# Kernel tuning notes

Hardware: AMD Instinct MI355X
Metric: run time of the kernel (lower is better)

Reference implementation:

```python
import jax, jax.numpy as jnp
import numpy as np

N = 100000          # total nodes (ground + sub)
G = 50000           # ground nodes (first G)
E = 800000          # edges per edge set
H = 64              # hidden_features
F_IN = 32           # node_features
MAX_DEG = 20        # MFConv max_degree
NUM_GRAPHS = 128
DEPTH = 1
LN_EPS = 1e-5


def setup_inputs() -> dict:
    key = jax.random.key(0)
    ks = jax.random.split(key, 12)

    def edges(k):
        return jax.random.randint(k, (2, E), 0, N, dtype=jnp.int32)

    return {
        "x": jax.random.normal(ks[0], (N, F_IN), jnp.float32),
        "edge_index": edges(ks[1]),
        "subgraph_edge_index": edges(ks[2]),
        "node_subnode_index": edges(ks[3]),
        "subnode_node_index": edges(ks[4]),
        "ground_node": jnp.arange(N) < G,
        "subgraph_batch_index": jax.random.randint(ks[5], (N - G,), 0, NUM_GRAPHS, dtype=jnp.int32),
        "batch_idx": jax.random.randint(ks[6], (N,), 0, NUM_GRAPHS, dtype=jnp.int32),
        # learned parameters
        "emb_w": jax.random.normal(ks[7], (F_IN, H), jnp.float32) / np.sqrt(F_IN).astype(np.float32),
        "emb_b": jnp.zeros((H,), jnp.float32),
        # 4 MFConvs per depth, 21 degree buckets each; lins_l has bias, lins_r has none
        "conv_wl": jax.random.normal(ks[8], (DEPTH, 4, MAX_DEG + 1, H, H), jnp.float32) / np.sqrt(H).astype(np.float32),
        "conv_bl": jnp.zeros((DEPTH, 4, MAX_DEG + 1, H), jnp.float32),
        "conv_wr": jax.random.normal(ks[9], (DEPTH, 4, MAX_DEG + 1, H, H), jnp.float32) / np.sqrt(H).astype(np.float32),
        "ln_g": jnp.ones((DEPTH, H), jnp.float32),
        "ln_b": jnp.zeros((DEPTH, H), jnp.float32),
        "out_w": jax.random.normal(ks[10], (H, 1), jnp.float32) / np.sqrt(H).astype(np.float32),
        "out_b": jnp.zeros((1,), jnp.float32),
    }


def _mfconv(x, ei, wl, bl, wr):
    """PyG MFConv: out_i = lins_l[deg_i](sum_{j->i} x_j) + lins_r[deg_i](x_i).
    Returns (out, update_mask) where update_mask marks nodes receiving >=1 message
    (catch_lone_sender equivalent)."""
    src, dst = ei[0], ei[1]
    n = x.shape[0]
    deg = jax.ops.segment_sum(jnp.ones(src.shape, jnp.float32), dst, num_segments=n)
    d = jnp.minimum(deg.astype(jnp.int32), MAX_DEG)
    h = jax.ops.segment_sum(x[src], dst, num_segments=n)      # [N, H] neighbor sum
    out = jnp.zeros_like(x)
    for k in range(MAX_DEG + 1):                              # fixed 21 degree buckets
        m = (d == k)[:, None]
        out = out + jnp.where(m, h @ wl[k] + bl[k] + x @ wr[k], 0.0)
    return out, deg > 0


def _layernorm(h, g, b):
    mu = jnp.mean(h, axis=-1, keepdims=True)
    var = jnp.mean(jnp.square(h - mu), axis=-1, keepdims=True)
    return (h - mu) * jax.lax.rsqrt(var + LN_EPS) * g + b


def reference(x, edge_index, subgraph_edge_index, node_subnode_index,
              subnode_node_index, ground_node, subgraph_batch_index, batch_idx,
              emb_w, emb_b, conv_wl, conv_bl, conv_wr, ln_g, ln_b, out_w, out_b):
    h = x @ emb_w + emb_b                                     # embedding
    eis = (edge_index, node_subnode_index, subgraph_edge_index, subnode_node_index)
    for i in range(DEPTH):
        if i != 0:
            h = jax.nn.relu(h)
        h0 = h                                                # residual skip
        for j, ei in enumerate(eis):
            out, upd = _mfconv(h, ei, conv_wl[i, j], conv_bl[i, j], conv_wr[i, j])
            h = jnp.where(upd[:, None], out, h)               # masking=True restore
            if j < 3:
                h = jax.nn.relu(h)
        h = _layernorm(h, ln_g[i], ln_b[i])
        h = h + h0
    # global_add_pool over ground nodes only
    pooled = jax.ops.segment_sum(jnp.where(ground_node[:, None], h, 0.0),
                                 batch_idx, num_segments=NUM_GRAPHS)
    return pooled @ out_w + out_b
```

## Files before the change

kernel.cpp:

```cpp
#include <hip/hip_runtime.h>

#define N_NODES 100000
#define G_NODES 50000
#define N_EDGES 800000
#define H 64
#define F_IN 32
#define MAX_DEG 20
#define NUM_GRAPHS 128
#define LN_EPS 1e-5f
#define POOL_BLOCKS 256
#define MAX_TILES 1600

#define NBINS 512
#define BPB 782
#define BINCAP_LOG 13
#define BINCAP 8192
#define CHUNK 6250
#define MKEYS (4 * N_NODES)
#define MEDGES (4 * N_EDGES)

typedef __attribute__((ext_vector_type(8))) short short8;
typedef __attribute__((ext_vector_type(4))) float float4v;

static __device__ __forceinline__ unsigned short f2b(float f) {
  unsigned u = __float_as_uint(f);
  return (unsigned short)((u + 0x7fffu + ((u >> 16) & 1u)) >> 16);
}
static __device__ __forceinline__ float b2f(unsigned short b) {
  return __uint_as_float(((unsigned)b) << 16);
}

__global__ __launch_bounds__(256) void wconv_kernel(
    const float* __restrict__ wl, const float* __restrict__ wr,
    const float* __restrict__ ew, unsigned short* __restrict__ wbt,
    unsigned short* __restrict__ ewbt, int* __restrict__ bincur,
    int* __restrict__ bcnt) {
  int i = blockIdx.x * 256 + threadIdx.x;
  if (blockIdx.x == 0) {
    for (int k = threadIdx.x; k < NBINS; k += 256) bincur[k] = k << BINCAP_LOG;
    if (threadIdx.x < 84) bcnt[threadIdx.x] = 0;
  }
  if (i < 84 * 64 * 128) {
    int k = i & 127;
    int ch = (i >> 7) & 63;
    int jb = i >> 13;
    float v = (k < 64) ? wl[jb * 4096 + k * 64 + ch]
                       : wr[jb * 4096 + (k - 64) * 64 + ch];
    wbt[i] = f2b(v);
  } else if (i < 84 * 64 * 128 + H * F_IN) {
    int ii = i - 84 * 64 * 128;
    int c = ii >> 5, f = ii & 31;
    ewbt[ii] = f2b(ew[f * H + c]);
  }
}

__global__ __launch_bounds__(256) void emb_kernel(
    const float* __restrict__ x, const unsigned short* __restrict__ ewbt,
    const float* __restrict__ eb, float* __restrict__ h0,
    unsigned short* __restrict__ ab, float* __restrict__ pooled) {
  int tid = threadIdx.x;
  if (blockIdx.x == 0) {
    for (int i = tid; i < NUM_GRAPHS * H; i += 256) pooled[i] = 0.f;
  }
  int base = blockIdx.x * 64;
  int nIn = min(64, N_NODES - base);
  int qw = tid >> 6, lane = tid & 63;
  __shared__ unsigned short aL[64 * 40];
  __shared__ float outF[64 * 68];

  {
    int node = tid >> 2, chb = (tid & 3) * 8;
    unsigned short v8[8];
    if (node < nIn) {
      const float* xr = x + ((size_t)(base + node)) * F_IN + chb;
      float4 f0 = *(const float4*)(xr);
      float4 f1 = *(const float4*)(xr + 4);
      v8[0] = f2b(f0.x); v8[1] = f2b(f0.y); v8[2] = f2b(f0.z); v8[3] = f2b(f0.w);
      v8[4] = f2b(f1.x); v8[5] = f2b(f1.y); v8[6] = f2b(f1.z); v8[7] = f2b(f1.w);
    } else {
#pragma unroll
      for (int i = 0; i < 8; ++i) v8[i] = 0;
    }
    *(short8*)&aL[(tid >> 2) * 40 + chb] = *(short8*)v8;
  }

  int m = lane & 15, quad = lane >> 4;
  short8 a = *(const short8*)&aL[(qw * 16 + m) * 40 + quad * 8];
  float4v acc[4];
#pragma unroll
  for (int t = 0; t < 4; ++t) {
    float bv = eb[t * 16 + m];
    acc[t] = (float4v){bv, bv, bv, bv};
  }
#pragma unroll
  for (int t = 0; t < 4; ++t) {
    short8 bf = *(const short8*)&ewbt[(t * 16 + m) * F_IN + quad * 8];
    acc[t] = __builtin_amdgcn_mfma_f32_16x16x32_bf16(a, bf, acc[t], 0, 0, 0);
  }
#pragma unroll
  for (int t = 0; t < 4; ++t)
#pragma unroll
    for (int r = 0; r < 4; ++r)
      outF[(qw * 16 + quad * 4 + r) * 68 + t * 16 + m] = acc[t][r];
  for (int r = qw * 16; r < qw * 16 + 16; ++r) {
    if (r < nIn) {
      int node = base + r;
      float v = outF[r * 68 + lane];
      if (node < G_NODES) h0[node * H + lane] = v;
      ab[node * 128 + 64 + lane] = f2b(v);
    }
  }
}

__global__ __launch_bounds__(1024) void p3_binscatter(
    const int* __restrict__ e0, const int* __restrict__ e1,
    const int* __restrict__ e2, const int* __restrict__ e3,
    int* __restrict__ bincur, unsigned* __restrict__ binned) {
  __shared__ int hist[NBINS];
  __shared__ int loff[NBINS];
  __shared__ int gcur[NBINS];
  __shared__ int lcur[NBINS];
  __shared__ int wtot[16];
  __shared__ int lmeta[CHUNK];
  __shared__ unsigned sbuf[CHUNK];
  __shared__ unsigned short sbin[CHUNK];
  int t = threadIdx.x, b = blockIdx.x;
  for (int i = t; i < NBINS; i += 1024) hist[i] = 0;
  __syncthreads();
  int j = b >> 7;
  const int* ei = (j == 0) ? e0 : (j == 1) ? e1 : (j == 2) ? e2 : e3;
  int ebase = (b & 127) * CHUNK;
  for (int i = t; i < CHUNK; i += 1024) {
    int dst = ei[N_EDGES + ebase + i];
    int key = j * N_NODES + dst;
    int bin = key / BPB;
    lmeta[i] = (bin << 10) | (key - bin * BPB);
    atomicAdd(&hist[bin], 1);
  }
  __syncthreads();
  int v = (t < NBINS) ? hist[t] : 0;
  int incl = v;
#pragma unroll
  for (int off = 1; off < 64; off <<= 1) {
    int y = __shfl_up(incl, off, 64);
    if ((t & 63) >= off) incl += y;
  }
  if (t < NBINS && (t & 63) == 63) wtot[t >> 6] = incl;
  __syncthreads();
  if (t < NBINS) {
    int wbase = 0;
    for (int w = 0; w < (t >> 6); ++w) wbase += wtot[w];
    int ex = wbase + incl - v;
    loff[t] = ex;
    lcur[t] = ex;
    gcur[t] = v ? atomicAdd(&bincur[t], v) : 0;
  }
  __syncthreads();
  for (int i = t; i < CHUNK; i += 1024) {
    int src = ei[ebase + i];
    int m = lmeta[i];
    int bin = m >> 10;
    int pos = atomicAdd(&lcur[bin], 1);
    sbuf[pos] = ((unsigned)(m & 1023) << 17) | (unsigned)src;
    sbin[pos] = (unsigned short)bin;
  }
  __syncthreads();
  for (int i = t; i < CHUNK; i += 1024) {
    int bb = sbin[i];
    binned[gcur[bb] + (i - loff[bb])] = sbuf[i];
  }
}

__global__ __launch_bounds__(1024) void p46_kernel(
    const unsigned* __restrict__ binned, const int* __restrict__ bincur,
    int* __restrict__ deg4, int* __restrict__ S, int* __restrict__ slots,
    int* __restrict__ bcnt) {
  __shared__ int hist[BPB];
  __shared__ int cur[BPB];
  __shared__ int bh[84];
  __shared__ int wtot[16];
  __shared__ unsigned bufin[BINCAP];
  __shared__ int bufout[BINCAP];
  int t = threadIdx.x, bin = blockIdx.x;
  int kb = bin * BPB;
  for (int i = t; i < BPB; i += 1024) hist[i] = 0;
  if (t < 84) bh[t] = 0;
  __syncthreads();
  int start = bin << BINCAP_LOG;
  int end = bincur[bin];
  int n = end - start;
  for (int i = t; i < n; i += 1024) {
    unsigned v = binned[start + i];
    bufin[i] = v;
    atomicAdd(&hist[v >> 17], 1);
  }
  __syncthreads();
  for (int i = t; i < BPB; i += 1024) {
    int key = kb + i;
    if (key < MKEYS) {
      int d = hist[i];
      deg4[key] = d;
      int j = key / N_NODES;
      int b = d < MAX_DEG ? d : MAX_DEG;
      atomicAdd(&bh[j * 21 + b], 1);
    }
  }
  int base = t * 4;
  int v0 = 0, v1 = 0, v2 = 0, v3 = 0;
  if (base < BPB) {
    v0 = hist[base];
    v1 = (base + 1 < BPB) ? hist[base + 1] : 0;
    v2 = (base + 2 < BPB) ? hist[base + 2] : 0;
    v3 = (base + 3 < BPB) ? hist[base + 3] : 0;
  }
  int s = v0 + v1 + v2 + v3;
  int incl = s;
#pragma unroll
  for (int off = 1; off < 64; off <<= 1) {
    int y = __shfl_up(incl, off, 64);
    if ((t & 63) >= off) incl += y;
  }
  if ((t & 63) == 63) wtot[t >> 6] = incl;
  __syncthreads();
  int wbase = 0;
  for (int w = 0; w < (t >> 6); ++w) wbase += wtot[w];
  int ex = wbase + incl - s;
  if (base < BPB) {
    cur[base] = ex;
    if (base + 1 < BPB) cur[base + 1] = ex + v0;
    if (base + 2 < BPB) cur[base + 2] = ex + v0 + v1;
    if (base + 3 < BPB) cur[base + 3] = ex + v0 + v1 + v2;
  }
  __syncthreads();
  for (int i = t; i < BPB; i += 1024)
    if (kb + i < MKEYS) S[kb + i] = start + cur[i];
  if (t < 84 && bh[t]) atomicAdd(&bcnt[t], bh[t]);
  __syncthreads();
  for (int i = t; i < n; i += 1024) {
    unsigned v = bufin[i];
    int pos = atomicAdd(&cur[v >> 17], 1);
    bufout[pos] = (int)(v & 0x1ffffu);
  }
  __syncthreads();
  for (int i = t; i < n; i += 1024) slots[start + i] = bufout[i];
}

__global__ __launch_bounds__(128) void bucket_scan(
    const int* __restrict__ bcnt, int* __restrict__ boff, int* __restrict__ bcur,
    int* __restrict__ ntiles, int* __restrict__ tdesc) {
  __shared__ int wt[2];
  __shared__ int exL[84], cntL[84], toffL[84];
  int t = threadIdx.x;
  int v = (t < 84) ? bcnt[t] : 0;
  int incl = v;
#pragma unroll
  for (int off = 1; off < 64; off <<= 1) {
    int y = __shfl_up(incl, off, 64);
    if ((t & 63) >= off) incl += y;
  }
  if ((t & 63) == 63) wt[t >> 6] = incl;
  __syncthreads();
  int wbase = (t >> 6) ? wt[0] : 0;
  if (t < 84) {
    int ex = wbase + incl - v;
    boff[t] = ex;
    bcur[t] = ex;
    exL[t] = ex;
    cntL[t] = v;
  }
  __syncthreads();
  if (t < 4) {
    int acc = 0;
    for (int bb = 0; bb < 21; ++bb) {
      toffL[t * 21 + bb] = acc;
      acc += (cntL[t * 21 + bb] + 63) >> 6;
    }
    ntiles[t] = acc;
  }
  __syncthreads();
  for (int jb = 0; jb < 84; ++jb) {
    int j = jb / 21, b = jb - j * 21;
    int cnt = cntL[jb], off = exL[jb], tb = toffL[jb];
    int nt = (cnt + 63) >> 6;
    for (int i = t; i < nt; i += 128) {
      int s2 = i << 6;
      int nIn = min(64, cnt - s2);
      tdesc[j * MAX_TILES + tb + i] = ((off + s2) << 12) | (b << 7) | nIn;
    }
  }
}

__global__ __launch_bounds__(256) void bucket_fill(
    const int* __restrict__ deg4, int* __restrict__ bcur, int* __restrict__ blist) {
  __shared__ int hist[21];
  __shared__ int base[21];
  int t = threadIdx.x;
  if (t < 21) hist[t] = 0;
  __syncthreads();
  int node = blockIdx.x * 256 + t;
  int j = blockIdx.y;
  int b = 0, lpos = 0;
  bool valid = (node < N_NODES);
  if (valid) {
    int d = deg4[j * N_NODES + node];
    b = d < MAX_DEG ? d : MAX_DEG;
    lpos = atomicAdd(&hist[b], 1);
  }
  __syncthreads();
  if (t < 21 && hist[t]) base[t] = atomicAdd(&bcur[j * 21 + t], hist[t]);
  __syncthreads();
  if (valid) blist[base[b] + lpos] = node;
}

__global__ __launch_bounds__(256) void conv_kernel(
    float* __restrict__ h, unsigned short* __restrict__ ab,
    const int* __restrict__ S, const int* __restrict__ deg,
    const int* __restrict__ slots,
    const int* __restrict__ blist, const int* __restrict__ tdesc,
    const int* __restrict__ ntiles, const unsigned short* __restrict__ wbt,
    const float* __restrict__ bl, int j, int inoff, int do_relu, int last) {
  if ((int)blockIdx.x >= ntiles[j]) return;
  int d = tdesc[j * MAX_TILES + blockIdx.x];
  int nIn = d & 127;
  int b = (d >> 7) & 31;
  const int* lst = blist + (d >> 12);
  int outoff = 64 - inoff;

  int tid = threadIdx.x;
  int qw = tid >> 6, lane = tid & 63;

  if (b == 0) {
    for (int r = qw * 16; r < qw * 16 + 16; ++r) {
      if (r < nIn) {
        int node = lst[r];
        float v = b2f(ab[node * 128 + inoff + lane]);
        if (do_relu) v = fmaxf(v, 0.f);
        if (last) {
          if (node < G_NODES) h[node * H + lane] = v;
        } else {
          ab[node * 128 + outoff + lane] = f2b(v);
        }
      }
    }
    return;
  }

  __shared__ unsigned short aL[64 * 136];
  __shared__ int nodeS[64];

  {
    int r = tid >> 2;
    int cb = (tid & 3) * 16;
    bool act = (r < nIn);
    int node = act ? lst[r] : 0;
    if ((tid & 3) == 0 && act) nodeS[r] = node;

    float acc[16];
#pragma unroll
    for (int k = 0; k < 16; ++k) acc[k] = 0.f;
    uint4 selfA = make_uint4(0u, 0u, 0u, 0u);
    uint4 selfB = make_uint4(0u, 0u, 0u, 0u);

#define ACC8(v, kb)                                                      \
  acc[kb + 0] += b2f((unsigned short)(v).x);                             \
  acc[kb + 1] += b2f((unsigned short)((v).x >> 16));                     \
  acc[kb + 2] += b2f((unsigned short)(v).y);                             \
  acc[kb + 3] += b2f((unsigned short)((v).y >> 16));                     \
  acc[kb + 4] += b2f((unsigned short)(v).z);                             \
  acc[kb + 5] += b2f((unsigned short)((v).z >> 16));                     \
  acc[kb + 6] += b2f((unsigned short)(v).w);                             \
  acc[kb + 7] += b2f((unsigned short)((v).w >> 16));

    if (act) {
      const unsigned short* abb = ab + inoff + cb;
      selfA = *(const uint4*)&abb[node * 128];
      selfB = *(const uint4*)&abb[node * 128 + 8];
      int off = S[node];
      int dg = (b < MAX_DEG) ? b : deg[node];
      int e = 0;
      for (; e + 3 < dg; e += 4) {
        int n0 = slots[off + e];
        int n1 = slots[off + e + 1];
        int n2 = slots[off + e + 2];
        int n3 = slots[off + e + 3];
        uint4 a0 = *(const uint4*)&abb[n0 * 128];
        uint4 b0 = *(const uint4*)&abb[n0 * 128 + 8];
        uint4 a1 = *(const uint4*)&abb[n1 * 128];
        uint4 b1 = *(const uint4*)&abb[n1 * 128 + 8];
        uint4 a2 = *(const uint4*)&abb[n2 * 128];
        uint4 b2 = *(const uint4*)&abb[n2 * 128 + 8];
        uint4 a3 = *(const uint4*)&abb[n3 * 128];
        uint4 b3 = *(const uint4*)&abb[n3 * 128 + 8];
        ACC8(a0, 0) ACC8(b0, 8)
        ACC8(a1, 0) ACC8(b1, 8)
        ACC8(a2, 0) ACC8(b2, 8)
        ACC8(a3, 0) ACC8(b3, 8)
      }
      int rem = dg - e;
      if (rem > 0) {
        int n0 = slots[off + e];
        int n1 = (rem > 1) ? slots[off + e + 1] : n0;
        int n2 = (rem > 2) ? slots[off + e + 2] : n0;
        uint4 a0 = *(const uint4*)&abb[n0 * 128];
        uint4 b0 = *(const uint4*)&abb[n0 * 128 + 8];
        uint4 a1 = *(const uint4*)&abb[n1 * 128];
        uint4 b1 = *(const uint4*)&abb[n1 * 128 + 8];
        uint4 a2 = *(const uint4*)&abb[n2 * 128];
        uint4 b2 = *(const uint4*)&abb[n2 * 128 + 8];
        ACC8(a0, 0) ACC8(b0, 8)
        if (rem > 1) { ACC8(a1, 0) ACC8(b1, 8) }
        if (rem > 2) { ACC8(a2, 0) ACC8(b2, 8) }
      }
    }
#undef ACC8

    unsigned p0 = (unsigned)f2b(acc[0]) | ((unsigned)f2b(acc[1]) << 16);
    unsigned p1 = (unsigned)f2b(acc[2]) | ((unsigned)f2b(acc[3]) << 16);
    unsigned p2 = (unsigned)f2b(acc[4]) | ((unsigned)f2b(acc[5]) << 16);
    unsigned p3 = (unsigned)f2b(acc[6]) | ((unsigned)f2b(acc[7]) << 16);
    unsigned p4 = (unsigned)f2b(acc[8]) | ((unsigned)f2b(acc[9]) << 16);
    unsigned p5 = (unsigned)f2b(acc[10]) | ((unsigned)f2b(acc[11]) << 16);
    unsigned p6 = (unsigned)f2b(acc[12]) | ((unsigned)f2b(acc[13]) << 16);
    unsigned p7 = (unsigned)f2b(acc[14]) | ((unsigned)f2b(acc[15]) << 16);
    *(uint4*)&aL[r * 136 + cb] = make_uint4(p0, p1, p2, p3);
    *(uint4*)&aL[r * 136 + cb + 8] = make_uint4(p4, p5, p6, p7);
    *(uint4*)&aL[r * 136 + 64 + cb] = selfA;
    *(uint4*)&aL[r * 136 + 64 + cb + 8] = selfB;
  }

  int m = lane & 15, quad = lane >> 4;
  const unsigned short* wbase = wbt + (size_t)(j * 21 + b) * 64 * 128;
  float4v acc[4];
#pragma unroll
  for (int t = 0; t < 4; ++t) {
    float bv = bl[b * 64 + t * 16 + m];
    acc[t] = (float4v){bv, bv, bv, bv};
  }
#pragma unroll
  for (int ks = 0; ks < 4; ++ks) {
    short8 a = *(const short8*)&aL[(qw * 16 + m) * 136 + ks * 32 + quad * 8];
#pragma unroll
    for (int t = 0; t < 4; ++t) {
      short8 bf = *(const short8*)&wbase[(t * 16 + m) * 128 + ks * 32 + quad * 8];
      acc[t] = __builtin_amdgcn_mfma_f32_16x16x32_bf16(a, bf, acc[t], 0, 0, 0);
    }
  }
  if (do_relu) {
#pragma unroll
    for (int t = 0; t < 4; ++t)
#pragma unroll
      for (int r = 0; r < 4; ++r) acc[t][r] = fmaxf(acc[t][r], 0.f);
  }
  float* outF = (float*)aL;
#pragma unroll
  for (int t = 0; t < 4; ++t)
#pragma unroll
    for (int r = 0; r < 4; ++r)
      outF[(qw * 16 + quad * 4 + r) * 68 + t * 16 + m] = acc[t][r];
  if (last) {
    for (int r = qw * 16; r < qw * 16 + 16; ++r)
      if (r < nIn && nodeS[r] < G_NODES)
        h[nodeS[r] * H + lane] = outF[r * 68 + lane];
  } else {
    for (int r = qw * 16; r < qw * 16 + 16; ++r)
      if (r < nIn) ab[nodeS[r] * 128 + outoff + lane] = f2b(outF[r * 68 + lane]);
  }
}

__global__ __launch_bounds__(1024) void ln_pool_kernel(
    const float* __restrict__ h, const float* __restrict__ h0,
    const float* __restrict__ g, const float* __restrict__ b,
    const int* __restrict__ batch, float* __restrict__ pooled) {
  __shared__ float sm[NUM_GRAPHS * H];
  int t = threadIdx.x;
  for (int i = t; i < NUM_GRAPHS * H; i += 1024) sm[i] = 0.f;
  __syncthreads();
  int lane = t & 63, w = t >> 6;
  const int per = (G_NODES + POOL_BLOCKS - 1) / POOL_BLOCKS;
  int start = blockIdx.x * per;
  int end = min(start + per, G_NODES);
  for (int node = start + w; node < end; node += 16) {
    int idx = node * H + lane;
    float v = h[idx];
    float s = v;
#pragma unroll
    for (int off = 32; off > 0; off >>= 1) s += __shfl_xor(s, off, 64);
    float mu = s * (1.0f / H);
    float dv = v - mu;
    float q = dv * dv;
#pragma unroll
    for (int off = 32; off > 0; off >>= 1) q += __shfl_xor(q, off, 64);
    float inv = rsqrtf(q * (1.0f / H) + LN_EPS);
    float r = dv * inv * g[lane] + b[lane] + h0[idx];
    atomicAdd(&sm[batch[node] * H + lane], r);
  }
  __syncthreads();
  for (int i = t; i < NUM_GRAPHS * H; i += 1024) {
    float v = sm[i];
    if (v != 0.f) atomicAdd(&pooled[i], v);
  }
}

__global__ __launch_bounds__(64) void out_kernel(
    const float* __restrict__ pooled, const float* __restrict__ w,
    const float* __restrict__ b, float* __restrict__ out) {
  int gph = blockIdx.x;
  int c = threadIdx.x;
  float v = pooled[gph * H + c] * w[c];
#pragma unroll
  for (int off = 32; off > 0; off >>= 1) v += __shfl_xor(v, off, 64);
  if (c == 0) out[gph] = v + b[0];
}

extern "C" void kernel_launch(void* const* d_in, const int* in_sizes, int n_in,
                              void* d_out, int out_size, void* d_ws, size_t ws_size,
                              hipStream_t stream) {
  const float* x       = (const float*)d_in[0];
  const int*   ei_edge = (const int*)d_in[1];
  const int*   ei_sub  = (const int*)d_in[2];
  const int*   ei_ns   = (const int*)d_in[3];
  const int*   ei_sn   = (const int*)d_in[4];
  const int*   batch   = (const int*)d_in[7];
  const float* emb_w   = (const float*)d_in[8];
  const float* emb_b   = (const float*)d_in[9];
  const float* conv_wl = (const float*)d_in[10];
  const float* conv_bl = (const float*)d_in[11];
  const float* conv_wr = (const float*)d_in[12];
  const float* ln_g    = (const float*)d_in[13];
  const float* ln_b    = (const float*)d_in[14];
  const float* out_w   = (const float*)d_in[15];
  const float* out_b   = (const float*)d_in[16];
  float* out = (float*)d_out;

  const size_t HB = (size_t)N_NODES * H * sizeof(float);
  char* ws = (char*)d_ws;
  float* h      = (float*)(ws);
  float* h0     = (float*)(ws + HB);
  unsigned short* ab = (unsigned short*)(ws + 2 * HB);
  int*   deg4   = (int*)(ws + 3 * HB);
  int*   S      = (int*)(ws + 78400000);
  int*   bcnt   = (int*)(ws + 92800000);
  int*   boff   = (int*)(ws + 92800512);
  int*   bcur   = (int*)(ws + 92801024);
  int*   blist  = (int*)(ws + 92801536);
  float* pooled = (float*)(ws + 94401536);
  unsigned short* wbt = (unsigned short*)(ws + 94434304);
  int*   tdesc  = (int*)(ws + 95810560);
  int*   ntiles = (int*)(ws + 95836160);
  unsigned short* ewbt = (unsigned short*)(ws + 95836608);
  int*   bincur = (int*)(ws + 95841024);
  unsigned* binned = (unsigned*)(ws + 100000000);
  int*   slots  = (int*)(ws + 117000000);

  const int* e0 = ei_edge, *e1 = ei_ns, *e2 = ei_sub, *e3 = ei_sn;

  wconv_kernel<<<(84 * 64 * 128 + H * F_IN + 255) / 256, 256, 0, stream>>>(
      conv_wl, conv_wr, emb_w, wbt, ewbt, bincur, bcnt);
  p3_binscatter<<<NBINS, 1024, 0, stream>>>(e0, e1, e2, e3, bincur, binned);
  p46_kernel<<<NBINS, 1024, 0, stream>>>(binned, bincur, deg4, S, slots, bcnt);
  bucket_scan<<<1, 128, 0, stream>>>(bcnt, boff, bcur, ntiles, tdesc);
  bucket_fill<<<dim3((N_NODES + 255) / 256, 4), 256, 0, stream>>>(deg4, bcur, blist);

  emb_kernel<<<(N_NODES + 63) / 64, 256, 0, stream>>>(x, ewbt, emb_b, h0, ab, pooled);

  for (int j = 0; j < 4; ++j) {
    conv_kernel<<<MAX_TILES, 256, 0, stream>>>(
        h, ab, S + j * N_NODES, deg4 + j * N_NODES, slots,
        blist, tdesc, ntiles, wbt,
        conv_bl + (size_t)j * 21 * H, j,
        (j & 1) ? 0 : 64,
        j < 3 ? 1 : 0, j == 3 ? 1 : 0);
  }

  ln_pool_kernel<<<POOL_BLOCKS, 1024, 0, stream>>>(h, h0, ln_g, ln_b, batch, pooled);
  out_kernel<<<NUM_GRAPHS, 64, 0, stream>>>(pooled, out_w, out_b, out);
}
```

Before: 334.4 us.

## Fuse weight conversion with embedding, unroll neighbor gather by 8, shrink pool grid

Merges the weight-conversion kernel and the embedding kernel into one launch. Embedding blocks now convert the fp32 embedding weights to bf16 inline instead of reading the pre-converted copy, which removes the dependency between the two. The conv kernel's neighbor gather gains an 8-way unrolled loop that keeps more independent loads in flight. The layernorm/pool grid is reduced from 256 to 96 blocks. These aim to cut launch overhead and gather latency, at the cost of redundant per-block weight conversion and higher register pressure in the gather.

Result: slower. 382.5 us (+14.4%).

```diff
diff --git a/kernel.cpp b/kernel.cpp
--- a/kernel.cpp
+++ b/kernel.cpp
@@ -8,7 +8,7 @@
 #define MAX_DEG 20
 #define NUM_GRAPHS 128
 #define LN_EPS 1e-5f
-#define POOL_BLOCKS 256
+#define POOL_BLOCKS 96
 #define MAX_TILES 1600
 
 #define NBINS 512
@@ -19,6 +19,9 @@
 #define MKEYS (4 * N_NODES)
 #define MEDGES (4 * N_EDGES)
 
+#define WCONV_BLOCKS 2688
+#define EMB_BLOCKS 1563
+
 typedef __attribute__((ext_vector_type(8))) short short8;
 typedef __attribute__((ext_vector_type(4))) float float4v;
 
@@ -30,39 +33,41 @@
   return __uint_as_float(((unsigned)b) << 16);
 }
 
-__global__ __launch_bounds__(256) void wconv_kernel(
+__global__ __launch_bounds__(256) void prep_kernel(
     const float* __restrict__ wl, const float* __restrict__ wr,
     const float* __restrict__ ew, unsigned short* __restrict__ wbt,
     unsigned short* __restrict__ ewbt, int* __restrict__ bincur,
-    int* __restrict__ bcnt) {
-  int i = blockIdx.x * 256 + threadIdx.x;
-  if (blockIdx.x == 0) {
-    for (int k = threadIdx.x; k < NBINS; k += 256) bincur[k] = k << BINCAP_LOG;
-    if (threadIdx.x < 84) bcnt[threadIdx.x] = 0;
-  }
-  if (i < 84 * 64 * 128) {
-    int k = i & 127;
-    int ch = (i >> 7) & 63;
-    int jb = i >> 13;
-    float v = (k < 64) ? wl[jb * 4096 + k * 64 + ch]
-                       : wr[jb * 4096 + (k - 64) * 64 + ch];
-    wbt[i] = f2b(v);
-  } else if (i < 84 * 64 * 128 + H * F_IN) {
-    int ii = i - 84 * 64 * 128;
-    int c = ii >> 5, f = ii & 31;
-    ewbt[ii] = f2b(ew[f * H + c]);
-  }
-}
-
-__global__ __launch_bounds__(256) void emb_kernel(
-    const float* __restrict__ x, const unsigned short* __restrict__ ewbt,
-    const float* __restrict__ eb, float* __restrict__ h0,
-    unsigned short* __restrict__ ab, float* __restrict__ pooled) {
+    int* __restrict__ bcnt,
+    const float* __restrict__ x, const float* __restrict__ eb,
+    float* __restrict__ h0, unsigned short* __restrict__ ab,
+    float* __restrict__ pooled) {
+  int bid = blockIdx.x;
   int tid = threadIdx.x;
-  if (blockIdx.x == 0) {
+  if (bid < WCONV_BLOCKS) {
+    int i = bid * 256 + tid;
+    if (bid == 0) {
+      for (int k = tid; k < NBINS; k += 256) bincur[k] = k << BINCAP_LOG;
+      if (tid < 84) bcnt[tid] = 0;
+    }
+    if (i < 84 * 64 * 128) {
+      int k = i & 127;
+      int ch = (i >> 7) & 63;
+      int jb = i >> 13;
+      float v = (k < 64) ? wl[jb * 4096 + k * 64 + ch]
+                         : wr[jb * 4096 + (k - 64) * 64 + ch];
+      wbt[i] = f2b(v);
+    } else if (i < 84 * 64 * 128 + H * F_IN) {
+      int ii = i - 84 * 64 * 128;
+      int c = ii >> 5, f = ii & 31;
+      ewbt[ii] = f2b(ew[f * H + c]);
+    }
+    return;
+  }
+  int ebid = bid - WCONV_BLOCKS;
+  if (ebid == 0) {
     for (int i = tid; i < NUM_GRAPHS * H; i += 256) pooled[i] = 0.f;
   }
-  int base = blockIdx.x * 64;
+  int base = ebid * 64;
   int nIn = min(64, N_NODES - base);
   int qw = tid >> 6, lane = tid & 63;
   __shared__ unsigned short aL[64 * 40];
@@ -94,7 +99,10 @@
   }
 #pragma unroll
   for (int t = 0; t < 4; ++t) {
-    short8 bf = *(const short8*)&ewbt[(t * 16 + m) * F_IN + quad * 8];
+    unsigned short bfv[8];
+#pragma unroll
+    for (int f = 0; f < 8; ++f) bfv[f] = f2b(ew[(quad * 8 + f) * H + t * 16 + m]);
+    short8 bf = *(short8*)bfv;
     acc[t] = __builtin_amdgcn_mfma_f32_16x16x32_bf16(a, bf, acc[t], 0, 0, 0);
   }
 #pragma unroll
@@ -378,6 +386,40 @@
       int off = S[node];
       int dg = (b < MAX_DEG) ? b : deg[node];
       int e = 0;
+      for (; e + 7 < dg; e += 8) {
+        int n0 = slots[off + e];
+        int n1 = slots[off + e + 1];
+        int n2 = slots[off + e + 2];
+        int n3 = slots[off + e + 3];
+        int n4 = slots[off + e + 4];
+        int n5 = slots[off + e + 5];
+        int n6 = slots[off + e + 6];
+        int n7 = slots[off + e + 7];
+        uint4 a0 = *(const uint4*)&abb[n0 * 128];
+        uint4 b0 = *(const uint4*)&abb[n0 * 128 + 8];
+        uint4 a1 = *(const uint4*)&abb[n1 * 128];
+        uint4 b1 = *(const uint4*)&abb[n1 * 128 + 8];
+        uint4 a2 = *(const uint4*)&abb[n2 * 128];
+        uint4 b2 = *(const uint4*)&abb[n2 * 128 + 8];
+        uint4 a3 = *(const uint4*)&abb[n3 * 128];
+        uint4 b3 = *(const uint4*)&abb[n3 * 128 + 8];
+        uint4 a4 = *(const uint4*)&abb[n4 * 128];
+        uint4 b4 = *(const uint4*)&abb[n4 * 128 + 8];
+        uint4 a5 = *(const uint4*)&abb[n5 * 128];
+        uint4 b5 = *(const uint4*)&abb[n5 * 128 + 8];
+        uint4 a6 = *(const uint4*)&abb[n6 * 128];
+        uint4 b6 = *(const uint4*)&abb[n6 * 128 + 8];
+        uint4 a7 = *(const uint4*)&abb[n7 * 128];
+        uint4 b7 = *(const uint4*)&abb[n7 * 128 + 8];
+        ACC8(a0, 0) ACC8(b0, 8)
+        ACC8(a1, 0) ACC8(b1, 8)
+        ACC8(a2, 0) ACC8(b2, 8)
+        ACC8(a3, 0) ACC8(b3, 8)
+        ACC8(a4, 0) ACC8(b4, 8)
+        ACC8(a5, 0) ACC8(b5, 8)
+        ACC8(a6, 0) ACC8(b6, 8)
+        ACC8(a7, 0) ACC8(b7, 8)
+      }
       for (; e + 3 < dg; e += 4) {
         int n0 = slots[off + e];
         int n1 = slots[off + e + 1];
@@ -554,14 +596,13 @@
 
   const int* e0 = ei_edge, *e1 = ei_ns, *e2 = ei_sub, *e3 = ei_sn;
 
-  wconv_kernel<<<(84 * 64 * 128 + H * F_IN + 255) / 256, 256, 0, stream>>>(
-      conv_wl, conv_wr, emb_w, wbt, ewbt, bincur, bcnt);
+  prep_kernel<<<WCONV_BLOCKS + EMB_BLOCKS, 256, 0, stream>>>(
+      conv_wl, conv_wr, emb_w, wbt, ewbt, bincur, bcnt,
+      x, emb_b, h0, ab, pooled);
   p3_binscatter<<<NBINS, 1024, 0, stream>>>(e0, e1, e2, e3, bincur, binned);
   p46_kernel<<<NBINS, 1024, 0, stream>>>(binned, bincur, deg4, S, slots, bcnt);
   bucket_scan<<<1, 128, 0, stream>>>(bcnt, boff, bcur, ntiles, tdesc);
   bucket_fill<<<dim3((N_NODES + 255) / 256, 4), 256, 0, stream>>>(deg4, bcur, blist);
-
-  emb_kernel<<<(N_NODES + 63) / 64, 256, 0, stream>>>(x, ewbt, emb_b, h0, ab, pooled);
 
   for (int j = 0; j < 4; ++j) {
     conv_kernel<<<MAX_TILES, 256, 0, stream>>>(
```
